# Optimization experiments

Measured on AMD Instinct MI355X. Metric: run time of the kernel, lower is better.

Reference implementation:

```python
import jax, jax.numpy as jnp
from jax import lax
import numpy as np

T, B, D = 24, 64, 1536
R, NUM_BLOCK = 5120, 5
NBN = R // NUM_BLOCK  # 1024 neurons per block
C = 100
THR_BASE = 0.5
REF_BASE = 0.5
Q0 = 0.8  # (100-20)/100 from wta_mem_update


@jax.custom_vjp
def spike_fn(v):
    # act_fun: heaviside forward, rectangular surrogate gradient
    return (v > 0).astype(v.dtype)

def _spike_fwd(v):
    return (v > 0).astype(v.dtype), v

def _spike_bwd(v, g):
    return (g * (jnp.abs(v) < 0.5).astype(g.dtype),)

spike_fn.defvjp(_spike_fwd, _spike_bwd)


def setup_inputs() -> dict:
    key = jax.random.key(0)
    ks = jax.random.split(key, 16)
    f32 = jnp.float32
    x = jax.random.normal(ks[0], (T, B, D), dtype=f32)
    Wp = jax.random.normal(ks[1], (R, D), dtype=f32) / np.sqrt(D)
    Wl = jax.random.normal(ks[2], (R, R), dtype=f32) / np.sqrt(R)
    Wm = jax.random.normal(ks[3], (C, R), dtype=f32) / np.sqrt(R)
    # adaptive LIF per-neuron parameters (as in __init__)
    decay = jax.random.uniform(ks[4], (R,), dtype=f32)
    thr_beta = 0.1 * jax.random.uniform(ks[5], (R,), dtype=f32)
    thr_decay = 0.5 * jax.random.uniform(ks[6], (R,), dtype=f32)
    ref_beta = 0.1 * jax.random.uniform(ks[7], (R,), dtype=f32)
    ref_decay = 0.5 * jax.random.uniform(ks[8], (R,), dtype=f32)
    cur_beta = 0.1 * jax.random.uniform(ks[9], (R,), dtype=f32)
    cur_decay = 0.5 * jax.random.uniform(ks[10], (R,), dtype=f32)
    # block-structured projection mask: [D, R] then transpose to weight layout [R, D]
    mask = np.zeros((D, R), dtype=np.float32)
    cum = np.cumsum([0, 512, 512, 256, 128])  # [0,512,1024,1280,1408]
    for i in range(len(cum) - 1):
        mask[cum[i]:cum[i + 1], NBN * i:NBN * (i + 1)] = 1.0
    proj_mask = jnp.asarray(mask.T)
    # sparse lateral mask: rand>0.8, no self-connection
    rng = np.random.RandomState(0)
    lat = (rng.rand(R, R) > 0.8).astype(np.float32)
    lat = lat * (1.0 - np.eye(R, dtype=np.float32))
    lat_mask = jnp.asarray(lat.T)
    return {
        "x": x, "ln_g": jnp.ones((D,), f32), "ln_b": jnp.zeros((D,), f32),
        "Wp": Wp, "bp": jnp.zeros((R,), f32), "Wl": Wl, "bl": jnp.zeros((R,), f32),
        "Wm": Wm, "bm": jnp.zeros((C,), f32),
        "decay": decay, "thr_beta": thr_beta, "thr_decay": thr_decay,
        "ref_beta": ref_beta, "ref_decay": ref_decay,
        "cur_beta": cur_beta, "cur_decay": cur_decay,
        "proj_mask": proj_mask, "lat_mask": lat_mask,
    }


def reference(x, ln_g, ln_b, Wp, bp, Wl, bl, Wm, bm,
              decay, thr_beta, thr_decay, ref_beta, ref_decay,
              cur_beta, cur_decay, proj_mask, lat_mask):
    Tn, Bn, Dn = x.shape
    Rn = Wp.shape[0]
    # parameter clamps done in forward of the torch module
    dec = jnp.clip(decay, 0.0, 1.0)
    thd = jnp.clip(thr_decay, 0.0, 1.0)
    rfd = jnp.clip(ref_decay, 0.0, 1.0)
    cud = jnp.clip(cur_decay, 0.0, 1.0)
    Wp_m = Wp * proj_mask       # masked feedforward projection
    Wl_m = Wl * lat_mask        # masked lateral recurrence
    # LayerNorm over fused multimodal features
    mu = x.mean(-1, keepdims=True)
    var = x.var(-1, keepdims=True)
    xn = (x - mu) * lax.rsqrt(var + 1e-5) * ln_g + ln_b
    # precompute feedforward drive for all steps: [T, B, R]
    drive = jnp.einsum('tbd,rd->tbr', xn, Wp_m) + bp

    def step(carry, dr_t):
        spike, mem, ttr, rtr, ctr, ssum = carry
        state = dr_t + spike @ Wl_m.T + bl
        thr = THR_BASE + thr_beta * ttr
        ref = REF_BASE + ref_beta * rtr
        cur = cur_beta * ctr
        mem = (mem - spike * ref) * dec + state + cur
        # WTA: quantile-threshold per group (torch row-major reshape [B, NBN, NUM_BLOCK])
        m3 = mem.reshape(Bn, NBN, NUM_BLOCK)
        nps = jnp.quantile(m3, Q0, axis=1, keepdims=True)
        mem = jax.nn.relu(m3 - nps).reshape(Bn, Rn)
        spk = spike_fn(mem - thr)
        ttr = ttr * thd + spk
        rtr = rtr * rfd + spk
        ctr = ctr * cud + spk
        return (spk, mem, ttr, rtr, ctr, ssum + spk), None

    z = jnp.zeros((Bn, Rn), x.dtype)
    (spk, mem, _, _, _, ssum), _ = lax.scan(step, (z, z, z, z, z, z), drive)
    # readout on time-averaged spike counts
    return (ssum / Tn) @ Wm.T + bm
```

## Files before the change

kernel.cpp:

```cpp
#include <hip/hip_runtime.h>
#include <math.h>

#define TSTEPS 24
#define BB 64
#define DD 1536
#define RR 5120
#define NB 5
#define CC 100
#define KS 2
#define WSCALE 67108864.0

typedef int i32x4 __attribute__((ext_vector_type(4)));

__device__ __forceinline__ int q_to_r(int q) { return (q & 1023) * 5 + (q >> 10); }

__device__ __forceinline__ unsigned fkey(float f) {
  unsigned u = __float_as_uint(f);
  return u ^ (((unsigned)((int)u >> 31)) | 0x80000000u);
}
__device__ __forceinline__ float fkeyinv(unsigned k) {
  unsigned u = (k & 0x80000000u) ? (k ^ 0x80000000u) : ~k;
  return __uint_as_float(u);
}

__global__ __launch_bounds__(256) void k_zero(float* __restrict__ state,
                                              unsigned* __restrict__ spike_i8_u32) {
  size_t n = 6ull * BB * RR;
  size_t nb = (size_t)BB * RR / 4;
  size_t gi = (size_t)blockIdx.x * 256 + threadIdx.x;
  for (size_t i = gi; i < n; i += (size_t)gridDim.x * 256) state[i] = 0.0f;
  for (size_t i = gi; i < nb; i += (size_t)gridDim.x * 256) spike_i8_u32[i] = 0u;
}

__global__ __launch_bounds__(256) void k_prep_params(
    const float* __restrict__ bp, const float* __restrict__ bl,
    const float* __restrict__ dec, const float* __restrict__ tb,
    const float* __restrict__ td, const float* __restrict__ rb,
    const float* __restrict__ rd, const float* __restrict__ cb,
    const float* __restrict__ cd, float* __restrict__ P) {
  int q = blockIdx.x * 256 + threadIdx.x;
  if (q >= RR) return;
  int r = q_to_r(q);
  P[0 * RR + q] = bp[r] + bl[r];
  P[1 * RR + q] = fminf(fmaxf(dec[r], 0.f), 1.f);
  P[2 * RR + q] = tb[r];
  P[3 * RR + q] = fminf(fmaxf(td[r], 0.f), 1.f);
  P[4 * RR + q] = rb[r];
  P[5 * RR + q] = fminf(fmaxf(rd[r], 0.f), 1.f);
  P[6 * RR + q] = cb[r];
  P[7 * RR + q] = fminf(fmaxf(cd[r], 0.f), 1.f);
}

__global__ __launch_bounds__(256) void k_prep_wm(const float* __restrict__ Wm,
                                                 float* __restrict__ Wmp) {
  int c = blockIdx.x;
  for (int q = threadIdx.x; q < RR; q += 256)
    Wmp[(size_t)c * RR + q] = Wm[(size_t)c * RR + q_to_r(q)];
}

__global__ __launch_bounds__(256) void k_prep_wpm(const float* __restrict__ Wp,
                                                  const float* __restrict__ pm,
                                                  float* __restrict__ Wpm) {
  int q = blockIdx.x;
  int r = q_to_r(q);
  const float* src = Wp + (size_t)r * DD;
  const float* msk = pm + (size_t)r * DD;
  float* dst = Wpm + (size_t)q * DD;
  for (int c = threadIdx.x; c < DD; c += 256) dst[c] = src[c] * msk[c];
}

__global__ __launch_bounds__(256) void k_build_wq_i8(const float* __restrict__ Wl,
                                                     const float* __restrict__ lmask,
                                                     signed char* __restrict__ Bd) {
  int qn = blockIdx.x;
  int rn = q_to_r(qn);
  const float* wr = Wl + (size_t)rn * RR;
  const float* mr = lmask + (size_t)rn * RR;
  size_t ob = (size_t)qn * RR;
  const size_t plane = (size_t)RR * RR;
  for (int qk = threadIdx.x; qk < RR; qk += 256) {
    int rk = q_to_r(qk);
    float w = wr[rk] * mr[rk];
    long long wi = llrint((double)w * WSCALE);
    int d0 = (int)(signed char)(wi & 0xFF);
    long long rem = (wi - d0) >> 8;
    int d1 = (int)(signed char)(rem & 0xFF);
    rem = (rem - d1) >> 8;
    Bd[ob + qk] = (signed char)d0;
    Bd[plane + ob + qk] = (signed char)d1;
    Bd[2 * plane + ob + qk] = (signed char)rem;
  }
}

__global__ __launch_bounds__(256) void k_layernorm(const float* __restrict__ x,
                                                   const float* __restrict__ g,
                                                   const float* __restrict__ be,
                                                   float* __restrict__ xn) {
  __shared__ float red[4];
  int row = blockIdx.x;
  int tid = threadIdx.x;
  const float* xr = x + (size_t)row * DD;
  float v[6];
  float s = 0.f;
#pragma unroll
  for (int i = 0; i < 6; i++) { v[i] = xr[i * 256 + tid]; s += v[i]; }
  for (int o = 32; o > 0; o >>= 1) s += __shfl_down(s, o, 64);
  int wv = tid >> 6, lane = tid & 63;
  if (lane == 0) red[wv] = s;
  __syncthreads();
  float mu = (red[0] + red[1] + red[2] + red[3]) * (1.0f / DD);
  __syncthreads();
  float sq = 0.f;
#pragma unroll
  for (int i = 0; i < 6; i++) { float d = v[i] - mu; sq += d * d; }
  for (int o = 32; o > 0; o >>= 1) sq += __shfl_down(sq, o, 64);
  if (lane == 0) red[wv] = sq;
  __syncthreads();
  float var = (red[0] + red[1] + red[2] + red[3]) * (1.0f / DD);
  float sc = 1.0f / sqrtf(var + 1e-5f);
#pragma unroll
  for (int i = 0; i < 6; i++) {
    int c = i * 256 + tid;
    xn[(size_t)row * DD + c] = (v[i] - mu) * sc * g[c] + be[c];
  }
}

__global__ __launch_bounds__(256) void k_gemm_drive(const float* __restrict__ A,
                                                    const float* __restrict__ Bw,
                                                    const float* __restrict__ bias,
                                                    float* __restrict__ Co) {
  __shared__ __align__(16) float As[16][68];
  __shared__ __align__(16) float Bs[16][68];
  int tid = threadIdx.x;
  int m0 = blockIdx.y * 64;
  int n0 = blockIdx.x * 64;
  int lr = tid >> 2;
  int lq = tid & 3;
  int tx = tid & 15;
  int ty = tid >> 4;
  float acc[4][4] = {};
  const float4* Arow = (const float4*)(A + (size_t)(m0 + lr) * DD);
  const float4* Brow = (const float4*)(Bw + (size_t)(n0 + lr) * DD);
  for (int k0 = 0; k0 < DD; k0 += 16) {
    float4 av = Arow[(k0 >> 2) + lq];
    float4 bv = Brow[(k0 >> 2) + lq];
    __syncthreads();
    As[lq * 4 + 0][lr] = av.x; As[lq * 4 + 1][lr] = av.y;
    As[lq * 4 + 2][lr] = av.z; As[lq * 4 + 3][lr] = av.w;
    Bs[lq * 4 + 0][lr] = bv.x; Bs[lq * 4 + 1][lr] = bv.y;
    Bs[lq * 4 + 2][lr] = bv.z; Bs[lq * 4 + 3][lr] = bv.w;
    __syncthreads();
#pragma unroll
    for (int kk = 0; kk < 16; kk++) {
      float4 a4 = *(const float4*)&As[kk][ty * 4];
      float4 b4 = *(const float4*)&Bs[kk][tx * 4];
      float av2[4] = {a4.x, a4.y, a4.z, a4.w};
      float bv2[4] = {b4.x, b4.y, b4.z, b4.w};
#pragma unroll
      for (int i2 = 0; i2 < 4; i2++)
#pragma unroll
        for (int j2 = 0; j2 < 4; j2++) acc[i2][j2] += av2[i2] * bv2[j2];
    }
  }
  float bb[4];
#pragma unroll
  for (int j2 = 0; j2 < 4; j2++) bb[j2] = bias[n0 + tx * 4 + j2];
#pragma unroll
  for (int i2 = 0; i2 < 4; i2++) {
    float4 o;
    o.x = acc[i2][0] + bb[0];
    o.y = acc[i2][1] + bb[1];
    o.z = acc[i2][2] + bb[2];
    o.w = acc[i2][3] + bb[3];
    *(float4*)(Co + (size_t)(m0 + ty * 4 + i2) * RR + n0 + tx * 4) = o;
  }
}

__global__ __launch_bounds__(256) void k_lat_gemm(const signed char* __restrict__ Asp,
                                                  const signed char* __restrict__ Bd,
                                                  long long* __restrict__ latp) {
  __shared__ long long lds[4][16][64];
  int tid = threadIdx.x;
  int lane = tid & 63;
  int w = tid >> 6;
  int n0 = blockIdx.x * 16;
  int ks = blockIdx.y;
  int k0 = ks * (RR / KS) + w * (RR / (KS * 4));
  int lm = lane & 15, lh = lane >> 4;
  const size_t plane = (size_t)RR * RR;
  i32x4 acc[4][3];
#pragma unroll
  for (int s = 0; s < 4; s++)
#pragma unroll
    for (int d = 0; d < 3; d++) acc[s][d] = (i32x4){0, 0, 0, 0};
  const i32x4* ap0 = (const i32x4*)(Asp + (size_t)(lm) * RR + k0 + lh * 16);
  const i32x4* ap1 = (const i32x4*)(Asp + (size_t)(16 + lm) * RR + k0 + lh * 16);
  const i32x4* ap2 = (const i32x4*)(Asp + (size_t)(32 + lm) * RR + k0 + lh * 16);
  const i32x4* ap3 = (const i32x4*)(Asp + (size_t)(48 + lm) * RR + k0 + lh * 16);
  const i32x4* bp0 = (const i32x4*)(Bd + (size_t)(n0 + lm) * RR + k0 + lh * 16);
  const i32x4* bp1 = (const i32x4*)(Bd + plane + (size_t)(n0 + lm) * RR + k0 + lh * 16);
  const i32x4* bp2 = (const i32x4*)(Bd + 2 * plane + (size_t)(n0 + lm) * RR + k0 + lh * 16);
#pragma unroll 2
  for (int kk = 0; kk < RR / (KS * 4 * 64); kk++) {
    i32x4 a0 = ap0[kk * 4];
    i32x4 a1 = ap1[kk * 4];
    i32x4 a2 = ap2[kk * 4];
    i32x4 a3 = ap3[kk * 4];
    i32x4 b0 = bp0[kk * 4];
    i32x4 b1 = bp1[kk * 4];
    i32x4 b2 = bp2[kk * 4];
    acc[0][0] = __builtin_amdgcn_mfma_i32_16x16x64_i8(a0, b0, acc[0][0], 0, 0, 0);
    acc[1][0] = __builtin_amdgcn_mfma_i32_16x16x64_i8(a1, b0, acc[1][0], 0, 0, 0);
    acc[2][0] = __builtin_amdgcn_mfma_i32_16x16x64_i8(a2, b0, acc[2][0], 0, 0, 0);
    acc[3][0] = __builtin_amdgcn_mfma_i32_16x16x64_i8(a3, b0, acc[3][0], 0, 0, 0);
    acc[0][1] = __builtin_amdgcn_mfma_i32_16x16x64_i8(a0, b1, acc[0][1], 0, 0, 0);
    acc[1][1] = __builtin_amdgcn_mfma_i32_16x16x64_i8(a1, b1, acc[1][1], 0, 0, 0);
    acc[2][1] = __builtin_amdgcn_mfma_i32_16x16x64_i8(a2, b1, acc[2][1], 0, 0, 0);
    acc[3][1] = __builtin_amdgcn_mfma_i32_16x16x64_i8(a3, b1, acc[3][1], 0, 0, 0);
    acc[0][2] = __builtin_amdgcn_mfma_i32_16x16x64_i8(a0, b2, acc[0][2], 0, 0, 0);
    acc[1][2] = __builtin_amdgcn_mfma_i32_16x16x64_i8(a1, b2, acc[1][2], 0, 0, 0);
    acc[2][2] = __builtin_amdgcn_mfma_i32_16x16x64_i8(a2, b2, acc[2][2], 0, 0, 0);
    acc[3][2] = __builtin_amdgcn_mfma_i32_16x16x64_i8(a3, b2, acc[3][2], 0, 0, 0);
  }
#pragma unroll
  for (int s = 0; s < 4; s++) {
#pragma unroll
    for (int r = 0; r < 4; r++) {
      long long v = (long long)acc[s][0][r]
                  + ((long long)acc[s][1][r] << 8)
                  + ((long long)acc[s][2][r] << 16);
      lds[w][s * 4 + r][lane] = v;
    }
  }
  __syncthreads();
  int o0 = tid * 4;
  int m = o0 >> 4;
  int ncb = o0 & 15;
  int s = m >> 4, lh2 = (m >> 2) & 3, rr = m & 3;
  long long* ob = latp + (size_t)ks * BB * RR + (size_t)m * RR + n0;
#pragma unroll
  for (int u = 0; u < 4; u++) {
    int nc = ncb + u;
    long long v = lds[0][s * 4 + rr][lh2 * 16 + nc]
                + lds[1][s * 4 + rr][lh2 * 16 + nc]
                + lds[2][s * 4 + rr][lh2 * 16 + nc]
                + lds[3][s * 4 + rr][lh2 * 16 + nc];
    ob[nc] = v;
  }
}

__global__ __launch_bounds__(256) void k_step(
    const float* __restrict__ drv_t,
    const long long* __restrict__ latp,
    const float* __restrict__ P,
    float* __restrict__ spike, float* __restrict__ memv,
    float* __restrict__ ttr, float* __restrict__ rtr, float* __restrict__ ctr,
    float* __restrict__ ssum, unsigned char* __restrict__ spike_i8) {
  __shared__ unsigned hist[256];
  __shared__ unsigned wtot[4];
  __shared__ unsigned s_prefix, s_rank, s_cle, s_min;

  int tid = threadIdx.x;
  int lane = tid & 63;
  int wv = tid >> 6;
  int j = blockIdx.x;
  int b = blockIdx.y;
  if (tid == 0) { s_prefix = 0u; s_rank = 818u; s_cle = 0u; s_min = 0xFFFFFFFFu; }

  size_t pbase4 = (size_t)b * RR + j * 1024 + 4 * tid;
  long long li[4] = {0, 0, 0, 0};
#pragma unroll
  for (int ks = 0; ks < KS; ks++) {
    const long long* p = latp + (size_t)ks * BB * RR + pbase4;
    li[0] += p[0]; li[1] += p[1]; li[2] += p[2]; li[3] += p[3];
  }
  float acc[4];
#pragma unroll
  for (int c = 0; c < 4; c++) acc[c] = (float)((double)li[c] * (1.0 / WSCALE));

  size_t sbase = pbase4;
  int pbase = j * 1024 + 4 * tid;
  float4 drv4 = *(const float4*)(drv_t + sbase);
  float4 mem4 = *(const float4*)(memv + sbase);
  float4 sp4 = *(const float4*)(spike + sbase);
  float4 tt4 = *(const float4*)(ttr + sbase);
  float4 tr4 = *(const float4*)(rtr + sbase);
  float4 tc4 = *(const float4*)(ctr + sbase);
  float4 dec4 = *(const float4*)(P + 1 * RR + pbase);
  float4 tb4 = *(const float4*)(P + 2 * RR + pbase);
  float4 rb4 = *(const float4*)(P + 4 * RR + pbase);
  float4 cb4 = *(const float4*)(P + 6 * RR + pbase);
  float mn[4], th[4];
  {
    const float* dv = (const float*)&drv4;
    const float* mv = (const float*)&mem4;
    const float* sv = (const float*)&sp4;
    const float* t1 = (const float*)&tt4;
    const float* t2 = (const float*)&tr4;
    const float* t3 = (const float*)&tc4;
    const float* dc = (const float*)&dec4;
    const float* b1 = (const float*)&tb4;
    const float* b2 = (const float*)&rb4;
    const float* b3 = (const float*)&cb4;
#pragma unroll
    for (int c = 0; c < 4; c++) {
      float rf = 0.5f + b2[c] * t2[c];
      float cu = b3[c] * t3[c];
      th[c] = 0.5f + b1[c] * t1[c];
      mn[c] = (mv[c] - sv[c] * rf) * dc[c] + (dv[c] + acc[c]) + cu;
    }
  }
  unsigned k4[4];
#pragma unroll
  for (int c = 0; c < 4; c++) k4[c] = fkey(mn[c]);

#pragma unroll
  for (int pass = 0; pass < 4; pass++) {
    int shift = 24 - pass * 8;
    unsigned maskhi = (pass == 0) ? 0u : (0xFFFFFFFFu << (shift + 8));
    hist[tid] = 0u;
    __syncthreads();
    unsigned pfx = s_prefix;
    unsigned rank = s_rank;
#pragma unroll
    for (int c = 0; c < 4; c++)
      if ((k4[c] & maskhi) == (pfx & maskhi)) atomicAdd(&hist[(k4[c] >> shift) & 255u], 1u);
    __syncthreads();
    unsigned cnt0 = hist[tid];
    unsigned v = cnt0;
    for (int o = 1; o < 64; o <<= 1) {
      unsigned n = (unsigned)__shfl_up((int)v, o, 64);
      if (lane >= o) v += n;
    }
    if (lane == 63) wtot[wv] = v;
    __syncthreads();
    unsigned add = 0;
    for (int w = 0; w < wv; w++) add += wtot[w];
    unsigned incl = v + add;
    unsigned excl = incl - cnt0;
    if (rank >= excl && rank < incl) {
      s_prefix = pfx | (((unsigned)tid) << shift);
      s_rank = rank - excl;
    }
    __syncthreads();
  }
  unsigned u818 = s_prefix;
  {
    int cl = 0;
    unsigned mnk = 0xFFFFFFFFu;
#pragma unroll
    for (int c = 0; c < 4; c++) {
      cl += (k4[c] <= u818) ? 1 : 0;
      if (k4[c] > u818) mnk = min(mnk, k4[c]);
    }
    atomicAdd(&s_cle, (unsigned)cl);
    atomicMin(&s_min, mnk);
  }
  __syncthreads();
  unsigned u819 = (s_cle >= 820u) ? u818 : s_min;
  float f818 = fkeyinv(u818), f819 = fkeyinv(u819);
  float nps = f818 + (0.8f * 1023.0f - 818.0f) * (f819 - f818);

  float4 td4 = *(const float4*)(P + 3 * RR + pbase);
  float4 rd4 = *(const float4*)(P + 5 * RR + pbase);
  float4 cd4 = *(const float4*)(P + 7 * RR + pbase);
  float4 ss4 = *(const float4*)(ssum + sbase);
  unsigned char si[4];
  {
    const float* d1 = (const float*)&td4;
    const float* d2 = (const float*)&rd4;
    const float* d3 = (const float*)&cd4;
    float* t1 = (float*)&tt4;
    float* t2 = (float*)&tr4;
    float* t3 = (float*)&tc4;
    float* sv = (float*)&sp4;
    float* mv = (float*)&mem4;
    float* ss = (float*)&ss4;
#pragma unroll
    for (int c = 0; c < 4; c++) {
      float mw = fmaxf(mn[c] - nps, 0.f);
      float sk = (mw - th[c] > 0.f) ? 1.f : 0.f;
      si[c] = (sk > 0.5f) ? (unsigned char)1 : (unsigned char)0;
      mv[c] = mw;
      t1[c] = t1[c] * d1[c] + sk;
      t2[c] = t2[c] * d2[c] + sk;
      t3[c] = t3[c] * d3[c] + sk;
      sv[c] = sk;
      ss[c] += sk;
    }
  }
  *(float4*)(memv + sbase) = mem4;
  *(float4*)(spike + sbase) = sp4;
  *(float4*)(ttr + sbase) = tt4;
  *(float4*)(rtr + sbase) = tr4;
  *(float4*)(ctr + sbase) = tc4;
  *(float4*)(ssum + sbase) = ss4;
  *(uchar4*)(spike_i8 + sbase) = make_uchar4(si[0], si[1], si[2], si[3]);
}

__global__ __launch_bounds__(256) void k_readout(const float* __restrict__ ssum,
                                                 const float* __restrict__ Wmp,
                                                 const float* __restrict__ bm,
                                                 float* __restrict__ out) {
  __shared__ float red[4];
  int c = blockIdx.x;
  int b = blockIdx.y;
  int tid = threadIdx.x;
  const float4* sp = (const float4*)(ssum + (size_t)b * RR);
  const float4* wp = (const float4*)(Wmp + (size_t)c * RR);
  float acc = 0.f;
#pragma unroll
  for (int i = 0; i < 5; i++) {
    float4 s4 = sp[i * 256 + tid];
    float4 w4 = wp[i * 256 + tid];
    acc += s4.x * w4.x + s4.y * w4.y + s4.z * w4.z + s4.w * w4.w;
  }
  for (int o = 32; o > 0; o >>= 1) acc += __shfl_down(acc, o, 64);
  if ((tid & 63) == 0) red[tid >> 6] = acc;
  __syncthreads();
  if (tid == 0)
    out[b * CC + c] = (red[0] + red[1] + red[2] + red[3]) * (1.0f / 24.0f) + bm[c];
}

extern "C" void kernel_launch(void* const* d_in, const int* in_sizes, int n_in,
                              void* d_out, int out_size, void* d_ws, size_t ws_size,
                              hipStream_t stream) {
  const float* x = (const float*)d_in[0];
  const float* ln_g = (const float*)d_in[1];
  const float* ln_b = (const float*)d_in[2];
  const float* Wp = (const float*)d_in[3];
  const float* bp = (const float*)d_in[4];
  const float* Wl = (const float*)d_in[5];
  const float* bl = (const float*)d_in[6];
  const float* Wm = (const float*)d_in[7];
  const float* bm = (const float*)d_in[8];
  const float* decay = (const float*)d_in[9];
  const float* thr_beta = (const float*)d_in[10];
  const float* thr_decay = (const float*)d_in[11];
  const float* ref_beta = (const float*)d_in[12];
  const float* ref_decay = (const float*)d_in[13];
  const float* cur_beta = (const float*)d_in[14];
  const float* cur_decay = (const float*)d_in[15];
  const float* proj_mask = (const float*)d_in[16];
  const float* lat_mask = (const float*)d_in[17];
  float* out = (float*)d_out;

  float* ws = (float*)d_ws;
  float* Wpm = ws;
  float* xn = Wpm + (size_t)RR * DD;
  float* drive = xn + (size_t)TSTEPS * BB * DD;
  float* state = drive + (size_t)TSTEPS * BB * RR;
  float* spike = state;
  float* memv = spike + (size_t)BB * RR;
  float* ttr = memv + (size_t)BB * RR;
  float* rtr = ttr + (size_t)BB * RR;
  float* ctr = rtr + (size_t)BB * RR;
  float* ssum = ctr + (size_t)BB * RR;
  float* P = ssum + (size_t)BB * RR;
  float* Wmp = P + 8 * RR;
  long long* latp = (long long*)(Wmp + (size_t)CC * RR);
  signed char* Bd = (signed char*)(latp + (size_t)KS * BB * RR);
  unsigned char* spike_i8 = (unsigned char*)(Bd + 3ull * RR * RR);

  hipLaunchKernelGGL(k_zero, dim3(512), dim3(256), 0, stream, state,
                     (unsigned*)spike_i8);
  hipLaunchKernelGGL(k_prep_params, dim3((RR + 255) / 256), dim3(256), 0, stream,
                     bp, bl, decay, thr_beta, thr_decay, ref_beta, ref_decay,
                     cur_beta, cur_decay, P);
  hipLaunchKernelGGL(k_prep_wm, dim3(CC), dim3(256), 0, stream, Wm, Wmp);
  hipLaunchKernelGGL(k_prep_wpm, dim3(RR), dim3(256), 0, stream, Wp, proj_mask, Wpm);
  hipLaunchKernelGGL(k_build_wq_i8, dim3(RR), dim3(256), 0, stream, Wl, lat_mask, Bd);
  hipLaunchKernelGGL(k_layernorm, dim3(TSTEPS * BB), dim3(256), 0, stream,
                     x, ln_g, ln_b, xn);
  hipLaunchKernelGGL(k_gemm_drive, dim3(RR / 64, TSTEPS * BB / 64), dim3(256), 0, stream,
                     xn, Wpm, P, drive);
  for (int t = 0; t < TSTEPS; t++) {
    hipLaunchKernelGGL(k_lat_gemm, dim3(RR / 16, KS), dim3(256), 0, stream,
                       (const signed char*)spike_i8, Bd, latp);
    hipLaunchKernelGGL(k_step, dim3(NB, BB), dim3(256), 0, stream,
                       drive + (size_t)t * BB * RR, latp, P,
                       spike, memv, ttr, rtr, ctr, ssum, spike_i8);
  }
  hipLaunchKernelGGL(k_readout, dim3(CC, BB), dim3(256), 0, stream, ssum, Wmp, bm, out);
}
```

Measured before the change: 1.437 ms.

## Fuse time-step loop into persistent kernel with grid barriers; enlarge drive GEMM tile

Replaces the 48 per-step kernel launches (lateral int8 MFMA GEMM plus WTA step) with one persistent kernel of 320 blocks. The blocks synchronise twice per step through an atomic-counter grid barrier, and the K split is removed so each block reduces the full K and writes float lateral input directly. This removes launch gaps and the partial-sum pass, but it depends on all 320 blocks being co-resident, otherwise it deadlocks. The drive GEMM also moves from 64x64 to 128x128 tiles with 8x8 register microtiles, to get more reuse per thread.

Result: slower. 3.019 ms (+110.1%).

```diff
diff --git a/kernel.cpp b/kernel.cpp
--- a/kernel.cpp
+++ b/kernel.cpp
@@ -7,7 +7,7 @@
 #define RR 5120
 #define NB 5
 #define CC 100
-#define KS 2
+#define NBLK (RR / 16)
 #define WSCALE 67108864.0
 
 typedef int i32x4 __attribute__((ext_vector_type(4)));
@@ -24,10 +24,12 @@
 }
 
 __global__ __launch_bounds__(256) void k_zero(float* __restrict__ state,
-                                              unsigned* __restrict__ spike_i8_u32) {
+                                              unsigned* __restrict__ spike_i8_u32,
+                                              unsigned* __restrict__ bar) {
   size_t n = 6ull * BB * RR;
   size_t nb = (size_t)BB * RR / 4;
   size_t gi = (size_t)blockIdx.x * 256 + threadIdx.x;
+  if (gi == 0) bar[0] = 0u;
   for (size_t i = gi; i < n; i += (size_t)gridDim.x * 256) state[i] = 0.0f;
   for (size_t i = gi; i < nb; i += (size_t)gridDim.x * 256) spike_i8_u32[i] = 0u;
 }
@@ -129,273 +131,299 @@
                                                     const float* __restrict__ Bw,
                                                     const float* __restrict__ bias,
                                                     float* __restrict__ Co) {
-  __shared__ __align__(16) float As[16][68];
-  __shared__ __align__(16) float Bs[16][68];
+  __shared__ __align__(16) float As[16][132];
+  __shared__ __align__(16) float Bs[16][132];
   int tid = threadIdx.x;
-  int m0 = blockIdx.y * 64;
-  int n0 = blockIdx.x * 64;
-  int lr = tid >> 2;
-  int lq = tid & 3;
+  int m0 = blockIdx.y * 128;
+  int n0 = blockIdx.x * 128;
+  int lr = tid >> 1;
+  int lhf = tid & 1;
   int tx = tid & 15;
   int ty = tid >> 4;
-  float acc[4][4] = {};
-  const float4* Arow = (const float4*)(A + (size_t)(m0 + lr) * DD);
-  const float4* Brow = (const float4*)(Bw + (size_t)(n0 + lr) * DD);
+  float acc[8][8] = {};
+  const float* Arow = A + (size_t)(m0 + lr) * DD + lhf * 8;
+  const float* Brow = Bw + (size_t)(n0 + lr) * DD + lhf * 8;
   for (int k0 = 0; k0 < DD; k0 += 16) {
-    float4 av = Arow[(k0 >> 2) + lq];
-    float4 bv = Brow[(k0 >> 2) + lq];
+    float4 a0 = *(const float4*)(Arow + k0);
+    float4 a1 = *(const float4*)(Arow + k0 + 4);
+    float4 b0 = *(const float4*)(Brow + k0);
+    float4 b1 = *(const float4*)(Brow + k0 + 4);
     __syncthreads();
-    As[lq * 4 + 0][lr] = av.x; As[lq * 4 + 1][lr] = av.y;
-    As[lq * 4 + 2][lr] = av.z; As[lq * 4 + 3][lr] = av.w;
-    Bs[lq * 4 + 0][lr] = bv.x; Bs[lq * 4 + 1][lr] = bv.y;
-    Bs[lq * 4 + 2][lr] = bv.z; Bs[lq * 4 + 3][lr] = bv.w;
+    As[lhf * 8 + 0][lr] = a0.x; As[lhf * 8 + 1][lr] = a0.y;
+    As[lhf * 8 + 2][lr] = a0.z; As[lhf * 8 + 3][lr] = a0.w;
+    As[lhf * 8 + 4][lr] = a1.x; As[lhf * 8 + 5][lr] = a1.y;
+    As[lhf * 8 + 6][lr] = a1.z; As[lhf * 8 + 7][lr] = a1.w;
+    Bs[lhf * 8 + 0][lr] = b0.x; Bs[lhf * 8 + 1][lr] = b0.y;
+    Bs[lhf * 8 + 2][lr] = b0.z; Bs[lhf * 8 + 3][lr] = b0.w;
+    Bs[lhf * 8 + 4][lr] = b1.x; Bs[lhf * 8 + 5][lr] = b1.y;
+    Bs[lhf * 8 + 6][lr] = b1.z; Bs[lhf * 8 + 7][lr] = b1.w;
     __syncthreads();
 #pragma unroll
     for (int kk = 0; kk < 16; kk++) {
-      float4 a4 = *(const float4*)&As[kk][ty * 4];
-      float4 b4 = *(const float4*)&Bs[kk][tx * 4];
-      float av2[4] = {a4.x, a4.y, a4.z, a4.w};
-      float bv2[4] = {b4.x, b4.y, b4.z, b4.w};
-#pragma unroll
-      for (int i2 = 0; i2 < 4; i2++)
-#pragma unroll
-        for (int j2 = 0; j2 < 4; j2++) acc[i2][j2] += av2[i2] * bv2[j2];
+      float4 x0 = *(const float4*)&As[kk][ty * 8];
+      float4 x1 = *(const float4*)&As[kk][ty * 8 + 4];
+      float4 y0 = *(const float4*)&Bs[kk][tx * 8];
+      float4 y1 = *(const float4*)&Bs[kk][tx * 8 + 4];
+      float av[8] = {x0.x, x0.y, x0.z, x0.w, x1.x, x1.y, x1.z, x1.w};
+      float bv[8] = {y0.x, y0.y, y0.z, y0.w, y1.x, y1.y, y1.z, y1.w};
+#pragma unroll
+      for (int i2 = 0; i2 < 8; i2++)
+#pragma unroll
+        for (int j2 = 0; j2 < 8; j2++) acc[i2][j2] += av[i2] * bv[j2];
     }
   }
-  float bb[4];
-#pragma unroll
-  for (int j2 = 0; j2 < 4; j2++) bb[j2] = bias[n0 + tx * 4 + j2];
-#pragma unroll
-  for (int i2 = 0; i2 < 4; i2++) {
-    float4 o;
-    o.x = acc[i2][0] + bb[0];
-    o.y = acc[i2][1] + bb[1];
-    o.z = acc[i2][2] + bb[2];
-    o.w = acc[i2][3] + bb[3];
-    *(float4*)(Co + (size_t)(m0 + ty * 4 + i2) * RR + n0 + tx * 4) = o;
+  float bb[8];
+#pragma unroll
+  for (int j2 = 0; j2 < 8; j2++) bb[j2] = bias[n0 + tx * 8 + j2];
+#pragma unroll
+  for (int i2 = 0; i2 < 8; i2++) {
+    float4 o0, o1;
+    o0.x = acc[i2][0] + bb[0]; o0.y = acc[i2][1] + bb[1];
+    o0.z = acc[i2][2] + bb[2]; o0.w = acc[i2][3] + bb[3];
+    o1.x = acc[i2][4] + bb[4]; o1.y = acc[i2][5] + bb[5];
+    o1.z = acc[i2][6] + bb[6]; o1.w = acc[i2][7] + bb[7];
+    float* orow = Co + (size_t)(m0 + ty * 8 + i2) * RR + n0 + tx * 8;
+    *(float4*)(orow) = o0;
+    *(float4*)(orow + 4) = o1;
   }
 }
 
-__global__ __launch_bounds__(256) void k_lat_gemm(const signed char* __restrict__ Asp,
-                                                  const signed char* __restrict__ Bd,
-                                                  long long* __restrict__ latp) {
-  __shared__ long long lds[4][16][64];
+struct ScanP {
+  const float* drive;
+  const signed char* Bd;
+  const float* P;
+  float* spike; float* memv; float* ttr; float* rtr; float* ctr; float* ssum;
+  unsigned char* spike_i8;
+  float* latf;
+  unsigned* bar;
+};
+
+__global__ __launch_bounds__(256, 2) void k_scan(ScanP p) {
+  __shared__ long long red64[4][16][64];
+  __shared__ unsigned hist[256];
+  __shared__ unsigned wtot[4];
+  __shared__ unsigned s_prefix, s_rank, s_cle, s_min;
+
+  const size_t plane = (size_t)RR * RR;
   int tid = threadIdx.x;
   int lane = tid & 63;
   int w = tid >> 6;
-  int n0 = blockIdx.x * 16;
-  int ks = blockIdx.y;
-  int k0 = ks * (RR / KS) + w * (RR / (KS * 4));
+  int bid = blockIdx.x;
   int lm = lane & 15, lh = lane >> 4;
-  const size_t plane = (size_t)RR * RR;
-  i32x4 acc[4][3];
-#pragma unroll
-  for (int s = 0; s < 4; s++)
-#pragma unroll
-    for (int d = 0; d < 3; d++) acc[s][d] = (i32x4){0, 0, 0, 0};
-  const i32x4* ap0 = (const i32x4*)(Asp + (size_t)(lm) * RR + k0 + lh * 16);
-  const i32x4* ap1 = (const i32x4*)(Asp + (size_t)(16 + lm) * RR + k0 + lh * 16);
-  const i32x4* ap2 = (const i32x4*)(Asp + (size_t)(32 + lm) * RR + k0 + lh * 16);
-  const i32x4* ap3 = (const i32x4*)(Asp + (size_t)(48 + lm) * RR + k0 + lh * 16);
-  const i32x4* bp0 = (const i32x4*)(Bd + (size_t)(n0 + lm) * RR + k0 + lh * 16);
-  const i32x4* bp1 = (const i32x4*)(Bd + plane + (size_t)(n0 + lm) * RR + k0 + lh * 16);
-  const i32x4* bp2 = (const i32x4*)(Bd + 2 * plane + (size_t)(n0 + lm) * RR + k0 + lh * 16);
+  unsigned bar_target = 0;
+
+  int n0 = bid * 16;
+  const i32x4* ap0 = (const i32x4*)((const signed char*)p.spike_i8 + (size_t)(lm) * RR + w * 1280 + lh * 16);
+  const i32x4* ap1 = (const i32x4*)((const signed char*)p.spike_i8 + (size_t)(16 + lm) * RR + w * 1280 + lh * 16);
+  const i32x4* ap2 = (const i32x4*)((const signed char*)p.spike_i8 + (size_t)(32 + lm) * RR + w * 1280 + lh * 16);
+  const i32x4* ap3 = (const i32x4*)((const signed char*)p.spike_i8 + (size_t)(48 + lm) * RR + w * 1280 + lh * 16);
+  const i32x4* bp0 = (const i32x4*)(p.Bd + (size_t)(n0 + lm) * RR + w * 1280 + lh * 16);
+  const i32x4* bp1 = (const i32x4*)(p.Bd + plane + (size_t)(n0 + lm) * RR + w * 1280 + lh * 16);
+  const i32x4* bp2 = (const i32x4*)(p.Bd + 2 * plane + (size_t)(n0 + lm) * RR + w * 1280 + lh * 16);
+
+  int j = bid % NB, b = bid / NB;
+  size_t pbase4 = (size_t)b * RR + j * 1024 + 4 * tid;
+  int pbase = j * 1024 + 4 * tid;
+
+#define GBAR()                                                            \
+  do {                                                                    \
+    __syncthreads();                                                      \
+    if (tid == 0) {                                                       \
+      __threadfence();                                                    \
+      atomicAdd(p.bar, 1u);                                               \
+      bar_target += (unsigned)NBLK;                                       \
+      while (atomicAdd(p.bar, 0u) < bar_target)                           \
+        __builtin_amdgcn_s_sleep(2);                                      \
+      __threadfence();                                                    \
+    }                                                                     \
+    __syncthreads();                                                      \
+  } while (0)
+
+  for (int t = 0; t < TSTEPS; ++t) {
+    {
+      i32x4 acc[4][3];
+#pragma unroll
+      for (int s = 0; s < 4; s++)
+#pragma unroll
+        for (int d = 0; d < 3; d++) acc[s][d] = (i32x4){0, 0, 0, 0};
 #pragma unroll 2
-  for (int kk = 0; kk < RR / (KS * 4 * 64); kk++) {
-    i32x4 a0 = ap0[kk * 4];
-    i32x4 a1 = ap1[kk * 4];
-    i32x4 a2 = ap2[kk * 4];
-    i32x4 a3 = ap3[kk * 4];
-    i32x4 b0 = bp0[kk * 4];
-    i32x4 b1 = bp1[kk * 4];
-    i32x4 b2 = bp2[kk * 4];
-    acc[0][0] = __builtin_amdgcn_mfma_i32_16x16x64_i8(a0, b0, acc[0][0], 0, 0, 0);
-    acc[1][0] = __builtin_amdgcn_mfma_i32_16x16x64_i8(a1, b0, acc[1][0], 0, 0, 0);
-    acc[2][0] = __builtin_amdgcn_mfma_i32_16x16x64_i8(a2, b0, acc[2][0], 0, 0, 0);
-    acc[3][0] = __builtin_amdgcn_mfma_i32_16x16x64_i8(a3, b0, acc[3][0], 0, 0, 0);
-    acc[0][1] = __builtin_amdgcn_mfma_i32_16x16x64_i8(a0, b1, acc[0][1], 0, 0, 0);
-    acc[1][1] = __builtin_amdgcn_mfma_i32_16x16x64_i8(a1, b1, acc[1][1], 0, 0, 0);
-    acc[2][1] = __builtin_amdgcn_mfma_i32_16x16x64_i8(a2, b1, acc[2][1], 0, 0, 0);
-    acc[3][1] = __builtin_amdgcn_mfma_i32_16x16x64_i8(a3, b1, acc[3][1], 0, 0, 0);
-    acc[0][2] = __builtin_amdgcn_mfma_i32_16x16x64_i8(a0, b2, acc[0][2], 0, 0, 0);
-    acc[1][2] = __builtin_amdgcn_mfma_i32_16x16x64_i8(a1, b2, acc[1][2], 0, 0, 0);
-    acc[2][2] = __builtin_amdgcn_mfma_i32_16x16x64_i8(a2, b2, acc[2][2], 0, 0, 0);
-    acc[3][2] = __builtin_amdgcn_mfma_i32_16x16x64_i8(a3, b2, acc[3][2], 0, 0, 0);
+      for (int kk = 0; kk < 20; kk++) {
+        i32x4 a0 = ap0[kk * 4];
+        i32x4 a1 = ap1[kk * 4];
+        i32x4 a2 = ap2[kk * 4];
+        i32x4 a3 = ap3[kk * 4];
+        i32x4 b0 = bp0[kk * 4];
+        i32x4 b1 = bp1[kk * 4];
+        i32x4 b2 = bp2[kk * 4];
+        acc[0][0] = __builtin_amdgcn_mfma_i32_16x16x64_i8(a0, b0, acc[0][0], 0, 0, 0);
+        acc[1][0] = __builtin_amdgcn_mfma_i32_16x16x64_i8(a1, b0, acc[1][0], 0, 0, 0);
+        acc[2][0] = __builtin_amdgcn_mfma_i32_16x16x64_i8(a2, b0, acc[2][0], 0, 0, 0);
+        acc[3][0] = __builtin_amdgcn_mfma_i32_16x16x64_i8(a3, b0, acc[3][0], 0, 0, 0);
+        acc[0][1] = __builtin_amdgcn_mfma_i32_16x16x64_i8(a0, b1, acc[0][1], 0, 0, 0);
+        acc[1][1] = __builtin_amdgcn_mfma_i32_16x16x64_i8(a1, b1, acc[1][1], 0, 0, 0);
+        acc[2][1] = __builtin_amdgcn_mfma_i32_16x16x64_i8(a2, b1, acc[2][1], 0, 0, 0);
+        acc[3][1] = __builtin_amdgcn_mfma_i32_16x16x64_i8(a3, b1, acc[3][1], 0, 0, 0);
+        acc[0][2] = __builtin_amdgcn_mfma_i32_16x16x64_i8(a0, b2, acc[0][2], 0, 0, 0);
+        acc[1][2] = __builtin_amdgcn_mfma_i32_16x16x64_i8(a1, b2, acc[1][2], 0, 0, 0);
+        acc[2][2] = __builtin_amdgcn_mfma_i32_16x16x64_i8(a2, b2, acc[2][2], 0, 0, 0);
+        acc[3][2] = __builtin_amdgcn_mfma_i32_16x16x64_i8(a3, b2, acc[3][2], 0, 0, 0);
+      }
+#pragma unroll
+      for (int s = 0; s < 4; s++) {
+#pragma unroll
+        for (int r = 0; r < 4; r++) {
+          long long v = (long long)acc[s][0][r]
+                      + ((long long)acc[s][1][r] << 8)
+                      + ((long long)acc[s][2][r] << 16);
+          red64[w][s * 4 + r][lane] = v;
+        }
+      }
+      __syncthreads();
+      int o0 = tid * 4;
+      int m = o0 >> 4;
+      int ncb = o0 & 15;
+      int ss = m >> 4, l2 = (m >> 2) & 3, rr2 = m & 3;
+      float* ob = p.latf + (size_t)m * RR + n0;
+#pragma unroll
+      for (int u = 0; u < 4; u++) {
+        int nc = ncb + u;
+        long long v = red64[0][ss * 4 + rr2][l2 * 16 + nc]
+                    + red64[1][ss * 4 + rr2][l2 * 16 + nc]
+                    + red64[2][ss * 4 + rr2][l2 * 16 + nc]
+                    + red64[3][ss * 4 + rr2][l2 * 16 + nc];
+        ob[nc] = (float)((double)v * (1.0 / WSCALE));
+      }
+    }
+    GBAR();
+    {
+      if (tid == 0) { s_prefix = 0u; s_rank = 818u; s_cle = 0u; s_min = 0xFFFFFFFFu; }
+      float accf[4];
+      {
+        float4 lv = *(const float4*)(p.latf + pbase4);
+        accf[0] = lv.x; accf[1] = lv.y; accf[2] = lv.z; accf[3] = lv.w;
+      }
+      size_t sbase = pbase4;
+      float4 drv4 = *(const float4*)(p.drive + (size_t)t * BB * RR + sbase);
+      float4 mem4 = *(const float4*)(p.memv + sbase);
+      float4 sp4 = *(const float4*)(p.spike + sbase);
+      float4 tt4 = *(const float4*)(p.ttr + sbase);
+      float4 tr4 = *(const float4*)(p.rtr + sbase);
+      float4 tc4 = *(const float4*)(p.ctr + sbase);
+      float4 dec4 = *(const float4*)(p.P + 1 * RR + pbase);
+      float4 tb4 = *(const float4*)(p.P + 2 * RR + pbase);
+      float4 rb4 = *(const float4*)(p.P + 4 * RR + pbase);
+      float4 cb4 = *(const float4*)(p.P + 6 * RR + pbase);
+      float mn[4], th[4];
+      {
+        const float* dv = (const float*)&drv4;
+        const float* mv = (const float*)&mem4;
+        const float* sv = (const float*)&sp4;
+        const float* t1 = (const float*)&tt4;
+        const float* t2 = (const float*)&tr4;
+        const float* t3 = (const float*)&tc4;
+        const float* dc = (const float*)&dec4;
+        const float* b1 = (const float*)&tb4;
+        const float* b2 = (const float*)&rb4;
+        const float* b3 = (const float*)&cb4;
+#pragma unroll
+        for (int c = 0; c < 4; c++) {
+          float rf = 0.5f + b2[c] * t2[c];
+          float cu = b3[c] * t3[c];
+          th[c] = 0.5f + b1[c] * t1[c];
+          mn[c] = (mv[c] - sv[c] * rf) * dc[c] + (dv[c] + accf[c]) + cu;
+        }
+      }
+      unsigned k4[4];
+#pragma unroll
+      for (int c = 0; c < 4; c++) k4[c] = fkey(mn[c]);
+
+#pragma unroll
+      for (int pass = 0; pass < 4; pass++) {
+        int shift = 24 - pass * 8;
+        unsigned maskhi = (pass == 0) ? 0u : (0xFFFFFFFFu << (shift + 8));
+        hist[tid] = 0u;
+        __syncthreads();
+        unsigned pfx = s_prefix;
+        unsigned rank = s_rank;
+#pragma unroll
+        for (int c = 0; c < 4; c++)
+          if ((k4[c] & maskhi) == (pfx & maskhi))
+            atomicAdd(&hist[(k4[c] >> shift) & 255u], 1u);
+        __syncthreads();
+        unsigned cnt0 = hist[tid];
+        unsigned v = cnt0;
+        for (int o = 1; o < 64; o <<= 1) {
+          unsigned nn = (unsigned)__shfl_up((int)v, o, 64);
+          if (lane >= o) v += nn;
+        }
+        if (lane == 63) wtot[w] = v;
+        __syncthreads();
+        unsigned add = 0;
+        for (int ww = 0; ww < w; ww++) add += wtot[ww];
+        unsigned incl = v + add;
+        unsigned excl = incl - cnt0;
+        if (rank >= excl && rank < incl) {
+          s_prefix = pfx | (((unsigned)tid) << shift);
+          s_rank = rank - excl;
+        }
+        __syncthreads();
+      }
+      unsigned u818 = s_prefix;
+      {
+        int cl = 0;
+        unsigned mnk = 0xFFFFFFFFu;
+#pragma unroll
+        for (int c = 0; c < 4; c++) {
+          cl += (k4[c] <= u818) ? 1 : 0;
+          if (k4[c] > u818) mnk = min(mnk, k4[c]);
+        }
+        atomicAdd(&s_cle, (unsigned)cl);
+        atomicMin(&s_min, mnk);
+      }
+      __syncthreads();
+      unsigned u819 = (s_cle >= 820u) ? u818 : s_min;
+      float f818 = fkeyinv(u818), f819 = fkeyinv(u819);
+      float nps = f818 + (0.8f * 1023.0f - 818.0f) * (f819 - f818);
+
+      float4 td4 = *(const float4*)(p.P + 3 * RR + pbase);
+      float4 rd4 = *(const float4*)(p.P + 5 * RR + pbase);
+      float4 cd4 = *(const float4*)(p.P + 7 * RR + pbase);
+      float4 ss4 = *(const float4*)(p.ssum + sbase);
+      unsigned char si[4];
+      {
+        const float* d1 = (const float*)&td4;
+        const float* d2 = (const float*)&rd4;
+        const float* d3 = (const float*)&cd4;
+        float* t1 = (float*)&tt4;
+        float* t2 = (float*)&tr4;
+        float* t3 = (float*)&tc4;
+        float* sv = (float*)&sp4;
+        float* mv = (float*)&mem4;
+        float* ss = (float*)&ss4;
+#pragma unroll
+        for (int c = 0; c < 4; c++) {
+          float mw = fmaxf(mn[c] - nps, 0.f);
+          float sk = (mw - th[c] > 0.f) ? 1.f : 0.f;
+          si[c] = (sk > 0.5f) ? (unsigned char)1 : (unsigned char)0;
+          mv[c] = mw;
+          t1[c] = t1[c] * d1[c] + sk;
+          t2[c] = t2[c] * d2[c] + sk;
+          t3[c] = t3[c] * d3[c] + sk;
+          sv[c] = sk;
+          ss[c] += sk;
+        }
+      }
+      *(float4*)(p.memv + sbase) = mem4;
+      *(float4*)(p.spike + sbase) = sp4;
+      *(float4*)(p.ttr + sbase) = tt4;
+      *(float4*)(p.rtr + sbase) = tr4;
+      *(float4*)(p.ctr + sbase) = tc4;
+      *(float4*)(p.ssum + sbase) = ss4;
+      *(uchar4*)(p.spike_i8 + sbase) = make_uchar4(si[0], si[1], si[2], si[3]);
+    }
+    GBAR();
   }
-#pragma unroll
-  for (int s = 0; s < 4; s++) {
-#pragma unroll
-    for (int r = 0; r < 4; r++) {
-      long long v = (long long)acc[s][0][r]
-                  + ((long long)acc[s][1][r] << 8)
-                  + ((long long)acc[s][2][r] << 16);
-      lds[w][s * 4 + r][lane] = v;
-    }
-  }
-  __syncthreads();
-  int o0 = tid * 4;
-  int m = o0 >> 4;
-  int ncb = o0 & 15;
-  int s = m >> 4, lh2 = (m >> 2) & 3, rr = m & 3;
-  long long* ob = latp + (size_t)ks * BB * RR + (size_t)m * RR + n0;
-#pragma unroll
-  for (int u = 0; u < 4; u++) {
-    int nc = ncb + u;
-    long long v = lds[0][s * 4 + rr][lh2 * 16 + nc]
-                + lds[1][s * 4 + rr][lh2 * 16 + nc]
-                + lds[2][s * 4 + rr][lh2 * 16 + nc]
-                + lds[3][s * 4 + rr][lh2 * 16 + nc];
-    ob[nc] = v;
-  }
-}
-
-__global__ __launch_bounds__(256) void k_step(
-    const float* __restrict__ drv_t,
-    const long long* __restrict__ latp,
-    const float* __restrict__ P,
-    float* __restrict__ spike, float* __restrict__ memv,
-    float* __restrict__ ttr, float* __restrict__ rtr, float* __restrict__ ctr,
-    float* __restrict__ ssum, unsigned char* __restrict__ spike_i8) {
-  __shared__ unsigned hist[256];
-  __shared__ unsigned wtot[4];
-  __shared__ unsigned s_prefix, s_rank, s_cle, s_min;
-
-  int tid = threadIdx.x;
-  int lane = tid & 63;
-  int wv = tid >> 6;
-  int j = blockIdx.x;
-  int b = blockIdx.y;
-  if (tid == 0) { s_prefix = 0u; s_rank = 818u; s_cle = 0u; s_min = 0xFFFFFFFFu; }
-
-  size_t pbase4 = (size_t)b * RR + j * 1024 + 4 * tid;
-  long long li[4] = {0, 0, 0, 0};
-#pragma unroll
-  for (int ks = 0; ks < KS; ks++) {
-    const long long* p = latp + (size_t)ks * BB * RR + pbase4;
-    li[0] += p[0]; li[1] += p[1]; li[2] += p[2]; li[3] += p[3];
-  }
-  float acc[4];
-#pragma unroll
-  for (int c = 0; c < 4; c++) acc[c] = (float)((double)li[c] * (1.0 / WSCALE));
-
-  size_t sbase = pbase4;
-  int pbase = j * 1024 + 4 * tid;
-  float4 drv4 = *(const float4*)(drv_t + sbase);
-  float4 mem4 = *(const float4*)(memv + sbase);
-  float4 sp4 = *(const float4*)(spike + sbase);
-  float4 tt4 = *(const float4*)(ttr + sbase);
-  float4 tr4 = *(const float4*)(rtr + sbase);
-  float4 tc4 = *(const float4*)(ctr + sbase);
-  float4 dec4 = *(const float4*)(P + 1 * RR + pbase);
-  float4 tb4 = *(const float4*)(P + 2 * RR + pbase);
-  float4 rb4 = *(const float4*)(P + 4 * RR + pbase);
-  float4 cb4 = *(const float4*)(P + 6 * RR + pbase);
-  float mn[4], th[4];
-  {
-    const float* dv = (const float*)&drv4;
-    const float* mv = (const float*)&mem4;
-    const float* sv = (const float*)&sp4;
-    const float* t1 = (const float*)&tt4;
-    const float* t2 = (const float*)&tr4;
-    const float* t3 = (const float*)&tc4;
-    const float* dc = (const float*)&dec4;
-    const float* b1 = (const float*)&tb4;
-    const float* b2 = (const float*)&rb4;
-    const float* b3 = (const float*)&cb4;
-#pragma unroll
-    for (int c = 0; c < 4; c++) {
-      float rf = 0.5f + b2[c] * t2[c];
-      float cu = b3[c] * t3[c];
-      th[c] = 0.5f + b1[c] * t1[c];
-      mn[c] = (mv[c] - sv[c] * rf) * dc[c] + (dv[c] + acc[c]) + cu;
-    }
-  }
-  unsigned k4[4];
-#pragma unroll
-  for (int c = 0; c < 4; c++) k4[c] = fkey(mn[c]);
-
-#pragma unroll
-  for (int pass = 0; pass < 4; pass++) {
-    int shift = 24 - pass * 8;
-    unsigned maskhi = (pass == 0) ? 0u : (0xFFFFFFFFu << (shift + 8));
-    hist[tid] = 0u;
-    __syncthreads();
-    unsigned pfx = s_prefix;
-    unsigned rank = s_rank;
-#pragma unroll
-    for (int c = 0; c < 4; c++)
-      if ((k4[c] & maskhi) == (pfx & maskhi)) atomicAdd(&hist[(k4[c] >> shift) & 255u], 1u);
-    __syncthreads();
-    unsigned cnt0 = hist[tid];
-    unsigned v = cnt0;
-    for (int o = 1; o < 64; o <<= 1) {
-      unsigned n = (unsigned)__shfl_up((int)v, o, 64);
-      if (lane >= o) v += n;
-    }
-    if (lane == 63) wtot[wv] = v;
-    __syncthreads();
-    unsigned add = 0;
-    for (int w = 0; w < wv; w++) add += wtot[w];
-    unsigned incl = v + add;
-    unsigned excl = incl - cnt0;
-    if (rank >= excl && rank < incl) {
-      s_prefix = pfx | (((unsigned)tid) << shift);
-      s_rank = rank - excl;
-    }
-    __syncthreads();
-  }
-  unsigned u818 = s_prefix;
-  {
-    int cl = 0;
-    unsigned mnk = 0xFFFFFFFFu;
-#pragma unroll
-    for (int c = 0; c < 4; c++) {
-      cl += (k4[c] <= u818) ? 1 : 0;
-      if (k4[c] > u818) mnk = min(mnk, k4[c]);
-    }
-    atomicAdd(&s_cle, (unsigned)cl);
-    atomicMin(&s_min, mnk);
-  }
-  __syncthreads();
-  unsigned u819 = (s_cle >= 820u) ? u818 : s_min;
-  float f818 = fkeyinv(u818), f819 = fkeyinv(u819);
-  float nps = f818 + (0.8f * 1023.0f - 818.0f) * (f819 - f818);
-
-  float4 td4 = *(const float4*)(P + 3 * RR + pbase);
-  float4 rd4 = *(const float4*)(P + 5 * RR + pbase);
-  float4 cd4 = *(const float4*)(P + 7 * RR + pbase);
-  float4 ss4 = *(const float4*)(ssum + sbase);
-  unsigned char si[4];
-  {
-    const float* d1 = (const float*)&td4;
-    const float* d2 = (const float*)&rd4;
-    const float* d3 = (const float*)&cd4;
-    float* t1 = (float*)&tt4;
-    float* t2 = (float*)&tr4;
-    float* t3 = (float*)&tc4;
-    float* sv = (float*)&sp4;
-    float* mv = (float*)&mem4;
-    float* ss = (float*)&ss4;
-#pragma unroll
-    for (int c = 0; c < 4; c++) {
-      float mw = fmaxf(mn[c] - nps, 0.f);
-      float sk = (mw - th[c] > 0.f) ? 1.f : 0.f;
-      si[c] = (sk > 0.5f) ? (unsigned char)1 : (unsigned char)0;
-      mv[c] = mw;
-      t1[c] = t1[c] * d1[c] + sk;
-      t2[c] = t2[c] * d2[c] + sk;
-      t3[c] = t3[c] * d3[c] + sk;
-      sv[c] = sk;
-      ss[c] += sk;
-    }
-  }
-  *(float4*)(memv + sbase) = mem4;
-  *(float4*)(spike + sbase) = sp4;
-  *(float4*)(ttr + sbase) = tt4;
-  *(float4*)(rtr + sbase) = tr4;
-  *(float4*)(ctr + sbase) = tc4;
-  *(float4*)(ssum + sbase) = ss4;
-  *(uchar4*)(spike_i8 + sbase) = make_uchar4(si[0], si[1], si[2], si[3]);
+#undef GBAR
 }
 
 __global__ __launch_bounds__(256) void k_readout(const float* __restrict__ ssum,
@@ -458,12 +486,13 @@
   float* ssum = ctr + (size_t)BB * RR;
   float* P = ssum + (size_t)BB * RR;
   float* Wmp = P + 8 * RR;
-  long long* latp = (long long*)(Wmp + (size_t)CC * RR);
-  signed char* Bd = (signed char*)(latp + (size_t)KS * BB * RR);
+  float* latf = Wmp + (size_t)CC * RR;
+  signed char* Bd = (signed char*)(latf + (size_t)BB * RR);
   unsigned char* spike_i8 = (unsigned char*)(Bd + 3ull * RR * RR);
+  unsigned* bar = (unsigned*)(spike_i8 + (size_t)BB * RR);
 
   hipLaunchKernelGGL(k_zero, dim3(512), dim3(256), 0, stream, state,
-                     (unsigned*)spike_i8);
+                     (unsigned*)spike_i8, bar);
   hipLaunchKernelGGL(k_prep_params, dim3((RR + 255) / 256), dim3(256), 0, stream,
                      bp, bl, decay, thr_beta, thr_decay, ref_beta, ref_decay,
                      cur_beta, cur_decay, P);
@@ -472,14 +501,23 @@
   hipLaunchKernelGGL(k_build_wq_i8, dim3(RR), dim3(256), 0, stream, Wl, lat_mask, Bd);
   hipLaunchKernelGGL(k_layernorm, dim3(TSTEPS * BB), dim3(256), 0, stream,
                      x, ln_g, ln_b, xn);
-  hipLaunchKernelGGL(k_gemm_drive, dim3(RR / 64, TSTEPS * BB / 64), dim3(256), 0, stream,
-                     xn, Wpm, P, drive);
-  for (int t = 0; t < TSTEPS; t++) {
-    hipLaunchKernelGGL(k_lat_gemm, dim3(RR / 16, KS), dim3(256), 0, stream,
-                       (const signed char*)spike_i8, Bd, latp);
-    hipLaunchKernelGGL(k_step, dim3(NB, BB), dim3(256), 0, stream,
-                       drive + (size_t)t * BB * RR, latp, P,
-                       spike, memv, ttr, rtr, ctr, ssum, spike_i8);
-  }
+  hipLaunchKernelGGL(k_gemm_drive, dim3(RR / 128, TSTEPS * BB / 128), dim3(256), 0,
+                     stream, xn, Wpm, P, drive);
+
+  ScanP sp_args;
+  sp_args.drive = drive;
+  sp_args.Bd = Bd;
+  sp_args.P = P;
+  sp_args.spike = spike;
+  sp_args.memv = memv;
+  sp_args.ttr = ttr;
+  sp_args.rtr = rtr;
+  sp_args.ctr = ctr;
+  sp_args.ssum = ssum;
+  sp_args.spike_i8 = spike_i8;
+  sp_args.latf = latf;
+  sp_args.bar = bar;
+  hipLaunchKernelGGL(k_scan, dim3(NBLK), dim3(256), 0, stream, sp_args);
+
   hipLaunchKernelGGL(k_readout, dim3(CC, BB), dim3(256), 0, stream, ssum, Wmp, bm, out);
 }
```
